# Optimization experiments

Measured on AMD Instinct MI355X. Metric: run time of the kernel, lower is better.

The kernel has to match this reference:

```python
import jax, jax.numpy as jnp
import numpy as np

B, T, N, CD, D = 8, 16, 256, 1280, 1024   # batch, frames, feats/frame, condition_dim, dim
H, DH, DEPTH, Q = 16, 64, 6, 16           # heads, dim_head, depth, latents per frame
FF = 4 * D


def setup_inputs() -> dict:
    key = jax.random.key(0)
    ks = iter(jax.random.split(key, 40))
    w = lambda shp: jax.random.normal(next(ks), shp, jnp.float32) * 0.02
    return dict(
        x_f=jax.random.normal(next(ks), (B, T, N, CD), jnp.float32),
        goal_w1=w((CD, 2 * D)), goal_b1=jnp.zeros((2 * D,), jnp.float32),
        goal_w2=w((2 * D, D)), goal_b2=jnp.zeros((D,), jnp.float32),
        latents=jax.random.normal(next(ks), (T, Q, D), jnp.float32),
        time_pos_emb=jax.random.normal(next(ks), (T, 1, D), jnp.float32),
        ln_media_g=jnp.ones((DEPTH, D), jnp.float32), ln_media_b=jnp.zeros((DEPTH, D), jnp.float32),
        ln_lat_g=jnp.ones((DEPTH, D), jnp.float32), ln_lat_b=jnp.zeros((DEPTH, D), jnp.float32),
        wq=w((DEPTH, D, H * DH)), wk=w((DEPTH, D, H * DH)), wv=w((DEPTH, D, H * DH)),
        wo=w((DEPTH, H * DH, D)),
        ffn_ln_g=jnp.ones((DEPTH, D), jnp.float32), ffn_ln_b=jnp.zeros((DEPTH, D), jnp.float32),
        ffn_w1=w((DEPTH, D, FF)), ffn_b1=jnp.zeros((DEPTH, FF), jnp.float32),
        ffn_w2=w((DEPTH, FF, D)), ffn_b2=jnp.zeros((DEPTH, D), jnp.float32),
        final_g=jnp.ones((D,), jnp.float32), final_b=jnp.zeros((D,), jnp.float32),
    )


def layer_norm(x, g, b, eps=1e-5):
    m = jnp.mean(x, axis=-1, keepdims=True)
    v = jnp.mean(jnp.square(x - m), axis=-1, keepdims=True)
    return (x - m) * jax.lax.rsqrt(v + eps) * g + b


def reference(x_f, goal_w1, goal_b1, goal_w2, goal_b2, latents, time_pos_emb,
              ln_media_g, ln_media_b, ln_lat_g, ln_lat_b, wq, wk, wv, wo,
              ffn_ln_g, ffn_ln_b, ffn_w1, ffn_b1, ffn_w2, ffn_b2, final_g, final_b):
    scale = DH ** -0.5
    # goal embedding: Linear -> GELU(exact) -> Linear, then add time positional embedding
    h = jax.nn.gelu(x_f @ goal_w1 + goal_b1, approximate=False) @ goal_w2 + goal_b2  # (B,T,N,D)
    h = h + time_pos_emb[None]                                                       # (T,1,D) broadcast
    feats = h.reshape(B * T, N, D)
    x = jnp.broadcast_to(latents[None], (B, T, Q, D)).reshape(B * T, Q, D)
    for i in range(DEPTH):
        f = layer_norm(feats, ln_media_g[i], ln_media_b[i])
        lat = layer_norm(x, ln_lat_g[i], ln_lat_b[i])
        q = (lat @ wq[i]).reshape(B * T, Q, H, DH).transpose(0, 2, 1, 3) * scale  # bhqd
        kv = jnp.concatenate([f, lat], axis=1)                                    # (BT, N+Q, D)
        k = (kv @ wk[i]).reshape(B * T, N + Q, H, DH).transpose(0, 2, 1, 3)       # bhfd
        v = (kv @ wv[i]).reshape(B * T, N + Q, H, DH).transpose(0, 2, 1, 3)
        sim = jnp.einsum('bhqd,bhfd->bhqf', q, k)
        alphas = jax.nn.softmax(sim, axis=-1)  # matches amax-subtract + softmax
        o = jnp.einsum('bhqf,bhfd->bhqd', alphas, v)
        o = o.transpose(0, 2, 1, 3).reshape(B * T, Q, H * DH)
        x = x + o @ wo[i]
        y = layer_norm(x, ffn_ln_g[i], ffn_ln_b[i])
        x = x + jax.nn.gelu(y @ ffn_w1[i] + ffn_b1[i], approximate=False) @ ffn_w2[i] + ffn_b2[i]
    x = x.reshape(B, T * Q, D)
    return layer_norm(x, final_g, final_b)
```

## Files before the change

### kernel.cpp

```cpp
#include <hip/hip_runtime.h>
#include <math.h>

#define DEV __device__ __forceinline__

typedef __attribute__((ext_vector_type(8))) short short8;
typedef __attribute__((ext_vector_type(4))) short short4v;
typedef __attribute__((ext_vector_type(4))) float f32x4;
typedef __attribute__((ext_vector_type(8))) __bf16 bf16x8;

DEV float bf2f(unsigned short u) {
    union { unsigned int i; float f; } c; c.i = ((unsigned int)u) << 16; return c.f;
}
DEV unsigned short f2bf(float f) {
    union { float f; unsigned int i; } c; c.f = f;
    unsigned int u = c.i;
    u += 0x7fffu + ((u >> 16) & 1u);
    return (unsigned short)(u >> 16);
}
DEV float gelu_exact(float x) { return 0.5f * x * (1.0f + erff(x * 0.70710678118654752f)); }

DEV f32x4 MF(bf16x8 a, bf16x8 b, f32x4 c) {
    return __builtin_amdgcn_mfma_f32_16x16x32_bf16(a, b, c, 0, 0, 0);
}

#define GLL16(g, l)                                                                   \
    __builtin_amdgcn_global_load_lds(                                                \
        (const __attribute__((address_space(1))) unsigned int*)(g),                  \
        (__attribute__((address_space(3))) unsigned int*)(l), 16, 0, 0)

#define BAR()     __builtin_amdgcn_s_barrier()
#define VMCNT(n)  asm volatile("s_waitcnt vmcnt(" #n ")" ::: "memory")
#define LGKM(n)   do { asm volatile("s_waitcnt lgkmcnt(" #n ")" ::: "memory");        \
                       __builtin_amdgcn_sched_barrier(0); } while (0)

__global__ __launch_bounds__(256)
void transpose_w(const float* __restrict__ in, unsigned short* __restrict__ out,
                 const float* __restrict__ rowscale, float uscale,
                 int K, int N, size_t inStride, size_t outStride, int scaleStride)
{
    __shared__ float tile[64][65];
    in  += (size_t)blockIdx.z * inStride;
    out += (size_t)blockIdx.z * outStride;
    const int k0 = blockIdx.y * 64, n0 = blockIdx.x * 64;
    const int tid = threadIdx.x;
    const int c = tid & 63;
#pragma unroll
    for (int i = 0; i < 16; ++i) {
        int rr = (i << 2) + (tid >> 6);
        float v = in[(size_t)(k0 + rr) * N + n0 + c];
        if (rowscale) v *= rowscale[(size_t)blockIdx.z * scaleStride + k0 + rr];
        tile[rr][c] = v * uscale;
    }
    __syncthreads();
#pragma unroll
    for (int i = 0; i < 16; ++i) {
        int rr = (i << 2) + (tid >> 6);
        out[(size_t)(n0 + rr) * K + k0 + c] = f2bf(tile[c][rr]);
    }
}

__global__ __launch_bounds__(256)
void fold_bias(const float* __restrict__ wk, const float* __restrict__ wv,
               const float* __restrict__ bmed, float* __restrict__ biaskv)
{
    const int d = blockIdx.x >> 3;
    const int rem = blockIdx.x & 7;
    const int part = rem >> 2;
    const int chunk = rem & 3;
    const float* w = (part ? wv : wk) + (size_t)d * 1024 * 1024 + chunk * 256 + threadIdx.x;
    const float* b = bmed + d * 1024;
    float acc = 0.f;
    for (int r = 0; r < 1024; ++r) acc += b[r] * w[(size_t)r * 1024];
    biaskv[d * 2048 + part * 1024 + chunk * 256 + threadIdx.x] = acc;
}

__global__ __launch_bounds__(256)
void convert_bf16(const float* __restrict__ in, unsigned short* __restrict__ out, size_t n4)
{
    size_t i = (size_t)blockIdx.x * 256 + threadIdx.x;
    if (i >= n4) return;
    float4 v = ((const float4*)in)[i];
    ushort4 u;
    u.x = f2bf(v.x); u.y = f2bf(v.y); u.z = f2bf(v.z); u.w = f2bf(v.w);
    ((ushort4*)out)[i] = u;
}

__global__ __launch_bounds__(256)
void init_x(const float* __restrict__ lat, float* __restrict__ x)
{
    const int row = blockIdx.x;
    ((float4*)x)[(size_t)row * 256 + threadIdx.x] =
        ((const float4*)lat)[(size_t)(row & 255) * 256 + threadIdx.x];
}

template<bool AFFINE, bool OUTBF>
__global__ __launch_bounds__(256)
void ln_k(const float* __restrict__ in, const float* __restrict__ g,
          const float* __restrict__ b, void* __restrict__ out)
{
    const int row = blockIdx.x;
    const int tid = threadIdx.x;
    float4 v = ((const float4*)(in + (size_t)row * 1024))[tid];
    float s  = v.x + v.y + v.z + v.w;
    float ss = v.x * v.x + v.y * v.y + v.z * v.z + v.w * v.w;
#pragma unroll
    for (int o = 32; o > 0; o >>= 1) { s += __shfl_down(s, o); ss += __shfl_down(ss, o); }
    __shared__ float red[8];
    if ((tid & 63) == 0) { red[tid >> 6] = s; red[4 + (tid >> 6)] = ss; }
    __syncthreads();
    const float sum  = red[0] + red[1] + red[2] + red[3];
    const float ssum = red[4] + red[5] + red[6] + red[7];
    const float mean = sum * (1.0f / 1024.0f);
    const float var  = ssum * (1.0f / 1024.0f) - mean * mean;
    const float rs   = rsqrtf(var + 1e-5f);
    float o0 = (v.x - mean) * rs, o1 = (v.y - mean) * rs;
    float o2 = (v.z - mean) * rs, o3 = (v.w - mean) * rs;
    if (AFFINE) {
        float4 gv = ((const float4*)g)[tid];
        float4 bv = ((const float4*)b)[tid];
        o0 = o0 * gv.x + bv.x; o1 = o1 * gv.y + bv.y;
        o2 = o2 * gv.z + bv.z; o3 = o3 * gv.w + bv.w;
    }
    if (OUTBF) {
        ushort4 u; u.x = f2bf(o0); u.y = f2bf(o1); u.z = f2bf(o2); u.w = f2bf(o3);
        ((ushort4*)out)[(size_t)row * 256 + tid] = u;
    } else {
        float4 ov; ov.x = o0; ov.y = o1; ov.z = o2; ov.w = o3;
        ((float4*)out)[(size_t)row * 256 + tid] = ov;
    }
}

enum { E_BF16 = 0, E_BIAS_BF16, E_BIAS_GELU_BF16, E_BIAS_TPOS_F32, E_ADD_F32, E_BIAS_ADD_F32 };

template<int EPI>
__global__ __launch_bounds__(512, 2)
void g8p(const unsigned short* __restrict__ A, const unsigned short* __restrict__ Bt,
         void* __restrict__ Out,
         const float* __restrict__ bias, const float* __restrict__ tpos,
         int M, int N, int K)
{
    __shared__ unsigned short sm[65536];

    const int tid = threadIdx.x;
    const int wid = tid >> 6, lane = tid & 63;
    const int wm = wid >> 2, wn = wid & 3;

    const int nbx = N >> 8;
    const int nwg = gridDim.x;
    const int bid = blockIdx.x;
    const int wg = (bid & 7) * (nwg >> 3) + (bid >> 3);
    const int by = wg / nbx, bx = wg % nbx;
    const int nt = K >> 6;

    const int srow = wid * 8 + (lane >> 3);
    const int schk = ((lane & 7) ^ (lane >> 3)) * 8;
    const unsigned short* gA = A  + (size_t)(by * 256 + srow) * K + schk;
    const unsigned short* gB = Bt + (size_t)(bx * 256 + srow) * K + schk;
    const int ldst = wid * 512;

    auto stgA = [&](int d, int h, int T) {
        const unsigned short* g = gA + (size_t)(h * 64) * K + (size_t)T * 64;
        unsigned short* l = sm + d * 16384 + h * 8192 + ldst;
        GLL16(g, l);
        GLL16(g + (size_t)128 * K, l + 4096);
    };
    auto stgB = [&](int d, int h, int T) {
        const unsigned short* g = gB + (size_t)(h * 128) * K + (size_t)T * 64;
        unsigned short* l = sm + 32768 + d * 16384 + h * 8192 + ldst;
        GLL16(g, l);
        GLL16(g + (size_t)64 * K, l + 4096);
    };

    const int q = lane >> 4;
    const int cks0 = ((q    ) ^ (lane & 7)) * 8;
    const int cks1 = ((q + 4) ^ (lane & 7)) * 8;
    const int arow = (wm * 64 + (lane & 15)) * 64;
    const int brow = ((wn & 1) * 64 + (lane & 15)) * 64;
    const int bhoff = 32768 + (wn >> 1) * 8192;

    f32x4 acc[8][4] = {};
    bf16x8 ax[2][2], ay[2][2], b[4][2];

#define READ_A(dst, base, HOFF, E0)                                                  \
    dst[0][0] = *(const bf16x8*)((base) + (HOFF) + arow + (E0) * 1024 + cks0);       \
    dst[0][1] = *(const bf16x8*)((base) + (HOFF) + arow + (E0) * 1024 + cks1);       \
    dst[1][0] = *(const bf16x8*)((base) + (HOFF) + arow + ((E0) + 1) * 1024 + cks0); \
    dst[1][1] = *(const bf16x8*)((base) + (HOFF) + arow + ((E0) + 1) * 1024 + cks1);

#define READ_Bm(Bb)                                                                  \
    _Pragma("unroll")                                                                \
    for (int ni = 0; ni < 4; ++ni) {                                                 \
        b[ni][0] = *(const bf16x8*)((Bb) + brow + ni * 1024 + cks0);                 \
        b[ni][1] = *(const bf16x8*)((Bb) + brow + ni * 1024 + cks1);                 \
    }

#define CLUST(R0, as)                                                                \
    __builtin_amdgcn_s_setprio(1);                                                   \
    _Pragma("unroll")                                                                \
    for (int e = 0; e < 2; ++e)                                                      \
        _Pragma("unroll")                                                            \
        for (int ni = 0; ni < 4; ++ni) {                                             \
            acc[(R0) + e][ni] = MF(as[e][0], b[ni][0], acc[(R0) + e][ni]);           \
            acc[(R0) + e][ni] = MF(as[e][1], b[ni][1], acc[(R0) + e][ni]);           \
        }                                                                            \
    __builtin_amdgcn_s_setprio(0);

    stgB(0, 0, 0); stgA(0, 0, 0); stgB(0, 1, 0); stgA(0, 1, 0);
    if (nt > 1) { stgB(1, 0, 1); stgA(1, 0, 1); }
    if (nt > 1) VMCNT(4); else VMCNT(0);
    BAR();
    READ_A(ax, sm, 0, 0);

    for (int T = 0; T < nt; ++T) {
        const int d = T & 1, dn = d ^ 1;
        const unsigned short* Ab  = sm + d * 16384;
        const unsigned short* Bb  = sm + bhoff + d * 16384;
        const unsigned short* AbN = sm + dn * 16384;
        const bool s1 = (T + 1 < nt), s2 = (T + 2 < nt);

        if (s1) { stgB(dn, 1, T + 1); stgA(dn, 1, T + 1); }
        READ_Bm(Bb);
        READ_A(ay, Ab, 0, 2);
        LGKM(4);
        CLUST(0, ax);
        BAR();

        if (s2) stgB(d, 0, T + 2);
        READ_A(ax, Ab, 8192, 0);
        LGKM(4);
        CLUST(2, ay);
        BAR();

        if (s2) stgA(d, 0, T + 2);
        READ_A(ay, Ab, 8192, 2);
        LGKM(4);
        CLUST(4, ax);

        if (s1) {
            if (s2) VMCNT(4); else VMCNT(0);
            BAR();
            READ_A(ax, AbN, 0, 0);
            LGKM(4);
        } else {
            LGKM(0);
        }
        CLUST(6, ay);
        BAR();
    }
#undef READ_A
#undef READ_Bm
#undef CLUST

    const int r0 = by * 256 + wm * 128 + (lane >> 4) * 4;
    const int c0 = bx * 256 + wn * 64 + (lane & 15);
#pragma unroll
    for (int mi = 0; mi < 8; ++mi) {
#pragma unroll
        for (int ni = 0; ni < 4; ++ni) {
            const int c = c0 + ni * 16;
            float bv = 0.f;
            if (EPI == E_BIAS_BF16 || EPI == E_BIAS_GELU_BF16 || EPI == E_BIAS_TPOS_F32)
                bv = bias[c];
#pragma unroll
            for (int j = 0; j < 4; ++j) {
                const int r = r0 + mi * 16 + j;
                float v = acc[mi][ni][j] + bv;
                if (EPI == E_BIAS_GELU_BF16) v = gelu_exact(v);
                if (EPI == E_BIAS_TPOS_F32) {
                    v += tpos[(((unsigned)r >> 8) & 15) * 1024 + c];
                    ((float*)Out)[(size_t)r * N + c] = v;
                } else {
                    ((unsigned short*)Out)[(size_t)r * N + c] = f2bf(v);
                }
            }
        }
    }
}

template<int EPI>
__global__ __launch_bounds__(256, 4)
void gemm64(const unsigned short* __restrict__ A, const unsigned short* __restrict__ Bt,
            void* __restrict__ Out,
            const float* __restrict__ bias, const float* __restrict__ addsrc,
            int M, int N, int K)
{
    __shared__ unsigned short lds[64 * 64 + 128 * 64];
    const int tid  = threadIdx.x;
    const int wave = tid >> 6, lane = tid & 63;
    const int nbx  = N >> 7;

    const int nwg = gridDim.x;
    int bid = blockIdx.x;
    int wg = ((nwg & 7) == 0) ? ((bid & 7) * (nwg >> 3) + (bid >> 3)) : bid;
    const int by = wg / nbx, bx = wg % nbx;

    const int swz = ((lane & 7) ^ (lane >> 3)) * 8;
    const unsigned short* gA = A  + (size_t)(by * 64  + (lane >> 3)) * K + swz;
    const unsigned short* gB = Bt + (size_t)(bx * 128 + (lane >> 3)) * K + swz;

    const int wr = wave >> 1, wc = wave & 1;
    f32x4 acc[2][4] = {};

    unsigned short* ldsA = lds;
    unsigned short* ldsB = lds + 64 * 64;

    const int off0 = (((lane >> 4)    ) ^ (lane & 7)) * 8;
    const int off1 = (((lane >> 4) | 4) ^ (lane & 7)) * 8;
    const unsigned short* la = ldsA + (wr * 32 + (lane & 15)) * 64;
    const unsigned short* lb = ldsB + (wc * 64 + (lane & 15)) * 64;

    for (int kt = 0; kt < K; kt += 64) {
        GLL16(gA + (size_t)(wave)     * 8 * K + kt, ldsA + (wave)      * 512);
        GLL16(gA + (size_t)(4 + wave) * 8 * K + kt, ldsA + (4 + wave)  * 512);
#pragma unroll
        for (int j = 0; j < 4; ++j) {
            const int chunk = (j << 2) + wave;
            GLL16(gB + (size_t)chunk * 8 * K + kt, ldsB + chunk * 512);
        }
        __syncthreads();
#pragma unroll
        for (int kk = 0; kk < 2; ++kk) {
            const int offk = kk ? off1 : off0;
            bf16x8 a[2], b[4];
#pragma unroll
            for (int m = 0; m < 2; ++m) a[m] = *(const bf16x8*)(la + m * 1024 + offk);
#pragma unroll
            for (int n = 0; n < 4; ++n) b[n] = *(const bf16x8*)(lb + n * 1024 + offk);
#pragma unroll
            for (int m = 0; m < 2; ++m)
#pragma unroll
                for (int n = 0; n < 4; ++n)
                    acc[m][n] = __builtin_amdgcn_mfma_f32_16x16x32_bf16(a[m], b[n], acc[m][n], 0, 0, 0);
        }
        __syncthreads();
    }

    const int r0 = by * 64 + wr * 32 + (lane >> 4) * 4;
    const int c0 = bx * 128 + wc * 64 + (lane & 15);
#pragma unroll
    for (int m = 0; m < 2; ++m) {
#pragma unroll
        for (int n = 0; n < 4; ++n) {
            const int c = c0 + n * 16;
#pragma unroll
            for (int j = 0; j < 4; ++j) {
                const int r = r0 + m * 16 + j;
                float v = acc[m][n][j];
                if (EPI == E_BIAS_BF16 || EPI == E_BIAS_GELU_BF16 || EPI == E_BIAS_ADD_F32)
                    v += bias[c];
                if (EPI == E_BIAS_GELU_BF16) v = gelu_exact(v);
                if (EPI == E_ADD_F32 || EPI == E_BIAS_ADD_F32) v += addsrc[(size_t)r * N + c];
                if (EPI == E_ADD_F32 || EPI == E_BIAS_ADD_F32)
                    ((float*)Out)[(size_t)r * N + c] = v;
                else
                    ((unsigned short*)Out)[(size_t)r * N + c] = f2bf(v);
            }
        }
    }
}

__global__ __launch_bounds__(256)
void attn_k(const unsigned short* __restrict__ qkvl, const unsigned short* __restrict__ kvm,
            unsigned short* __restrict__ o)
{
    __shared__ unsigned short kv[272 * 72];
    __shared__ float sim[16 * 273];
    __shared__ float qs[16 * 68];
    __shared__ float red[64];

    const int bt = blockIdx.x >> 4, h = blockIdx.x & 15;
    const int tid = threadIdx.x;
    const int lane = tid & 63, wave = tid >> 6;
    const int r = tid & 15, grp = tid >> 4;

    {
        const int qi = tid >> 4, d0 = (tid & 15) * 4;
        const unsigned short* src = qkvl + (size_t)(bt * 16 + qi) * 3072 + h * 64 + d0;
        qs[qi * 68 + d0 + 0] = bf2f(src[0]);
        qs[qi * 68 + d0 + 1] = bf2f(src[1]);
        qs[qi * 68 + d0 + 2] = bf2f(src[2]);
        qs[qi * 68 + d0 + 3] = bf2f(src[3]);
    }
#pragma unroll
    for (int i = 0; i < 9; ++i) {
        int idx = i * 256 + tid;
        if (idx < 2176) {
            int f = idx >> 3, cp = idx & 7;
            const unsigned short* src = (f < 256)
                ? kvm  + (size_t)(bt * 256 + f) * 2048 + h * 64 + cp * 8
                : qkvl + (size_t)(bt * 16 + (f - 256)) * 3072 + 1024 + h * 64 + cp * 8;
            *(short8*)&kv[f * 72 + cp * 8] = *(const short8*)src;
        }
    }
    __syncthreads();

    float p[17];
#pragma unroll
    for (int i = 0; i < 17; ++i) p[i] = 0.f;
#pragma unroll
    for (int d = 0; d < 64; d += 8) {
        float q8[8];
#pragma unroll
        for (int j = 0; j < 8; ++j) q8[j] = qs[r * 68 + d + j];
#pragma unroll
        for (int i = 0; i < 17; ++i) {
            short8 k8 = *(const short8*)&kv[(grp + i * 16) * 72 + d];
#pragma unroll
            for (int j = 0; j < 8; ++j) p[i] += q8[j] * bf2f((unsigned short)k8[j]);
        }
    }
    float mx = -3.0e38f;
#pragma unroll
    for (int i = 0; i < 17; ++i) mx = fmaxf(mx, p[i]);
    mx = fmaxf(mx, __shfl_xor(mx, 16));
    mx = fmaxf(mx, __shfl_xor(mx, 32));
    if (lane < 16) red[wave * 16 + lane] = mx;
    __syncthreads();
    const float rowmax = fmaxf(fmaxf(red[r], red[16 + r]), fmaxf(red[32 + r], red[48 + r]));

    float sm = 0.f;
#pragma unroll
    for (int i = 0; i < 17; ++i) { p[i] = __expf(p[i] - rowmax); sm += p[i]; }
    sm += __shfl_xor(sm, 16);
    sm += __shfl_xor(sm, 32);
#pragma unroll
    for (int i = 0; i < 17; ++i) sim[r * 273 + grp + i * 16] = p[i];
    __syncthreads();
    if (lane < 16) red[wave * 16 + lane] = sm;
#pragma unroll
    for (int i = 0; i < 9; ++i) {
        int idx = i * 256 + tid;
        if (idx < 2176) {
            int f = idx >> 3, cp = idx & 7;
            const unsigned short* src = (f < 256)
                ? kvm  + (size_t)(bt * 256 + f) * 2048 + 1024 + h * 64 + cp * 8
                : qkvl + (size_t)(bt * 16 + (f - 256)) * 3072 + 2048 + h * 64 + cp * 8;
            *(short8*)&kv[f * 72 + cp * 8] = *(const short8*)src;
        }
    }
    __syncthreads();
    const float inv = 1.0f / (red[r] + red[16 + r] + red[32 + r] + red[48 + r]);

    float o0 = 0.f, o1 = 0.f, o2 = 0.f, o3 = 0.f;
    for (int f = 0; f < 272; ++f) {
        float pv = sim[r * 273 + f];
        short4v v4 = *(const short4v*)&kv[f * 72 + grp * 4];
        o0 += pv * bf2f((unsigned short)v4[0]);
        o1 += pv * bf2f((unsigned short)v4[1]);
        o2 += pv * bf2f((unsigned short)v4[2]);
        o3 += pv * bf2f((unsigned short)v4[3]);
    }
    unsigned short* dst = o + (size_t)(bt * 16 + r) * 1024 + h * 64 + grp * 4;
    dst[0] = f2bf(o0 * inv);
    dst[1] = f2bf(o1 * inv);
    dst[2] = f2bf(o2 * inv);
    dst[3] = f2bf(o3 * inv);
}

extern "C" void kernel_launch(void* const* d_in, const int* in_sizes, int n_in,
                              void* d_out, int out_size, void* d_ws, size_t ws_size,
                              hipStream_t stream)
{
    const float* x_f      = (const float*)d_in[0];
    const float* goal_w1  = (const float*)d_in[1];
    const float* goal_b1  = (const float*)d_in[2];
    const float* goal_w2  = (const float*)d_in[3];
    const float* goal_b2  = (const float*)d_in[4];
    const float* latents  = (const float*)d_in[5];
    const float* tpos     = (const float*)d_in[6];
    const float* lnm_g    = (const float*)d_in[7];
    const float* lnm_b    = (const float*)d_in[8];
    const float* lnl_g    = (const float*)d_in[9];
    const float* lnl_b    = (const float*)d_in[10];
    const float* wq       = (const float*)d_in[11];
    const float* wk       = (const float*)d_in[12];
    const float* wv       = (const float*)d_in[13];
    const float* wo       = (const float*)d_in[14];
    const float* ffn_g    = (const float*)d_in[15];
    const float* ffn_b    = (const float*)d_in[16];
    const float* ffw1     = (const float*)d_in[17];
    const float* ffb1     = (const float*)d_in[18];
    const float* ffw2     = (const float*)d_in[19];
    const float* ffb2     = (const float*)d_in[20];
    const float* fin_g    = (const float*)d_in[21];
    const float* fin_b    = (const float*)d_in[22];

    char* ws = (char*)d_ws;
    size_t off = 0;
    auto alloc = [&](size_t bytes) -> char* {
        char* p = ws + off;
        off += (bytes + 255) & ~(size_t)255;
        return p;
    };
    typedef unsigned short u16;
    u16*   wg1t   = (u16*)  alloc(2048ull * 1280 * 2);
    u16*   wg2t   = (u16*)  alloc(1024ull * 2048 * 2);
    u16*   wqkvl  = (u16*)  alloc(6ull * 3072 * 1024 * 2);
    u16*   wkvm   = (u16*)  alloc(6ull * 2048 * 1024 * 2);
    u16*   wot    = (u16*)  alloc(6ull * 1024 * 1024 * 2);
    u16*   wf1t   = (u16*)  alloc(6ull * 4096 * 1024 * 2);
    u16*   wf2t   = (u16*)  alloc(6ull * 1024 * 4096 * 2);
    float* biaskv = (float*)alloc(6ull * 2048 * 4);
    float* xres   = (float*)alloc(2048ull * 1024 * 4);
    u16*   latn   = (u16*)  alloc(2048ull * 1024 * 2);
    u16*   qkvl   = (u16*)  alloc(2048ull * 3072 * 2);
    u16*   obuf   = (u16*)  alloc(2048ull * 1024 * 2);
    u16*   ffny   = (u16*)  alloc(2048ull * 1024 * 2);
    u16*   ffnmid = (u16*)  alloc(2048ull * 4096 * 2);
    u16*   bufA   = (u16*)  alloc(32768ull * 2048 * 2);
    float* bufB   = (float*)alloc(32768ull * 1024 * 4);
    u16*   bufC   = (u16*)  alloc(41943040ull * 2);
    if (off > ws_size) return;

    convert_bf16<<<40960, 256, 0, stream>>>(x_f, bufC, 41943040ull / 4);
    transpose_w<<<dim3(32, 20, 1), 256, 0, stream>>>(goal_w1, wg1t, nullptr, 1.f, 1280, 2048, 0, 0, 0);
    transpose_w<<<dim3(16, 32, 1), 256, 0, stream>>>(goal_w2, wg2t, nullptr, 1.f, 2048, 1024, 0, 0, 0);
    transpose_w<<<dim3(16, 16, 6), 256, 0, stream>>>(wq, wqkvl,                nullptr, 0.125f, 1024, 1024, 1024ull*1024, 3072ull*1024, 0);
    transpose_w<<<dim3(16, 16, 6), 256, 0, stream>>>(wk, wqkvl + 1024ull*1024, nullptr, 1.f,    1024, 1024, 1024ull*1024, 3072ull*1024, 0);
    transpose_w<<<dim3(16, 16, 6), 256, 0, stream>>>(wv, wqkvl + 2048ull*1024, nullptr, 1.f,    1024, 1024, 1024ull*1024, 3072ull*1024, 0);
    transpose_w<<<dim3(16, 16, 6), 256, 0, stream>>>(wk, wkvm,                 lnm_g,   1.f,    1024, 1024, 1024ull*1024, 2048ull*1024, 1024);
    transpose_w<<<dim3(16, 16, 6), 256, 0, stream>>>(wv, wkvm + 1024ull*1024,  lnm_g,   1.f,    1024, 1024, 1024ull*1024, 2048ull*1024, 1024);
    transpose_w<<<dim3(16, 16, 6), 256, 0, stream>>>(wo, wot,                  nullptr, 1.f,    1024, 1024, 1024ull*1024, 1024ull*1024, 0);
    transpose_w<<<dim3(64, 16, 6), 256, 0, stream>>>(ffw1, wf1t,               nullptr, 1.f,    1024, 4096, 4096ull*1024, 4096ull*1024, 0);
    transpose_w<<<dim3(16, 64, 6), 256, 0, stream>>>(ffw2, wf2t,               nullptr, 1.f,    4096, 1024, 4096ull*1024, 4096ull*1024, 0);
    fold_bias<<<48, 256, 0, stream>>>(wk, wv, lnm_b, biaskv);
    init_x<<<2048, 256, 0, stream>>>(latents, xres);

    g8p<E_BIAS_GELU_BF16><<<1024, 512, 0, stream>>>(bufC, wg1t, bufA, goal_b1, nullptr, 32768, 2048, 1280);
    g8p<E_BIAS_TPOS_F32><<<512, 512, 0, stream>>>(bufA, wg2t, bufB, goal_b2, tpos, 32768, 1024, 2048);
    ln_k<false, true><<<32768, 256, 0, stream>>>(bufB, nullptr, nullptr, bufC);

    for (int i = 0; i < 6; ++i) {
        const u16* wqkvl_i = wqkvl + (size_t)i * 3072 * 1024;
        const u16* wkvm_i  = wkvm  + (size_t)i * 2048 * 1024;
        const u16* wot_i   = wot   + (size_t)i * 1024 * 1024;
        const u16* wf1_i   = wf1t  + (size_t)i * 4096 * 1024;
        const u16* wf2_i   = wf2t  + (size_t)i * 1024 * 4096;

        ln_k<true, true><<<2048, 256, 0, stream>>>(xres, lnl_g + i * 1024, lnl_b + i * 1024, latn);
        gemm64<E_BF16><<<32 * 24, 256, 0, stream>>>(latn, wqkvl_i, qkvl, nullptr, nullptr, 2048, 3072, 1024);
        g8p<E_BIAS_BF16><<<1024, 512, 0, stream>>>(bufC, wkvm_i, bufA, biaskv + i * 2048, nullptr, 32768, 2048, 1024);
        attn_k<<<2048, 256, 0, stream>>>(qkvl, bufA, obuf);
        gemm64<E_ADD_F32><<<32 * 8, 256, 0, stream>>>(obuf, wot_i, xres, nullptr, xres, 2048, 1024, 1024);
        ln_k<true, true><<<2048, 256, 0, stream>>>(xres, ffn_g + i * 1024, ffn_b + i * 1024, ffny);
        gemm64<E_BIAS_GELU_BF16><<<32 * 32, 256, 0, stream>>>(ffny, wf1_i, ffnmid, ffb1 + i * 4096, nullptr, 2048, 4096, 1024);
        gemm64<E_BIAS_ADD_F32><<<32 * 8, 256, 0, stream>>>(ffnmid, wf2_i, xres, ffb2 + i * 1024, xres, 2048, 1024, 4096);
    }

    ln_k<true, false><<<2048, 256, 0, stream>>>(xres, fin_g, fin_b, d_out);
}
```

Before: 2.727 ms.

## Restructure GEMM main loop with ping-pong B registers and one barrier per tile

Rewrites the large-tile GEMM K-loop as a two-way unrolled TILE macro. B fragments alternate between two register sets, so the next tile's B and A can be read right after a single barrier and overlap with the last MFMA cluster. This removes the three extra barriers per tile of the old schedule. In exchange, global prefetch depth drops from two tiles ahead to one, with a full vmcnt(0) wait every tile, and register pressure rises from the extra B buffer. The unroll assumes an even tile count, which the model's K sizes satisfy.

```diff
diff --git a/kernel.cpp b/kernel.cpp
--- a/kernel.cpp
+++ b/kernel.cpp
@@ -179,7 +179,7 @@
     const int bhoff = 32768 + (wn >> 1) * 8192;
 
     f32x4 acc[8][4] = {};
-    bf16x8 ax[2][2], ay[2][2], b[4][2];
+    bf16x8 aX[2][2], aY[2][2], b0[4][2], b1[4][2];
 
 #define READ_A(dst, base, HOFF, E0)                                                  \
     dst[0][0] = *(const bf16x8*)((base) + (HOFF) + arow + (E0) * 1024 + cks0);       \
@@ -187,69 +187,70 @@
     dst[1][0] = *(const bf16x8*)((base) + (HOFF) + arow + ((E0) + 1) * 1024 + cks0); \
     dst[1][1] = *(const bf16x8*)((base) + (HOFF) + arow + ((E0) + 1) * 1024 + cks1);
 
-#define READ_Bm(Bb)                                                                  \
+#define READ_B(dst, Bb)                                                              \
     _Pragma("unroll")                                                                \
     for (int ni = 0; ni < 4; ++ni) {                                                 \
-        b[ni][0] = *(const bf16x8*)((Bb) + brow + ni * 1024 + cks0);                 \
-        b[ni][1] = *(const bf16x8*)((Bb) + brow + ni * 1024 + cks1);                 \
-    }
-
-#define CLUST(R0, as)                                                                \
+        dst[ni][0] = *(const bf16x8*)((Bb) + brow + ni * 1024 + cks0);               \
+        dst[ni][1] = *(const bf16x8*)((Bb) + brow + ni * 1024 + cks1);               \
+    }
+
+#define CLUST(R0, AS, BS)                                                            \
     __builtin_amdgcn_s_setprio(1);                                                   \
     _Pragma("unroll")                                                                \
     for (int e = 0; e < 2; ++e)                                                      \
         _Pragma("unroll")                                                            \
         for (int ni = 0; ni < 4; ++ni) {                                             \
-            acc[(R0) + e][ni] = MF(as[e][0], b[ni][0], acc[(R0) + e][ni]);           \
-            acc[(R0) + e][ni] = MF(as[e][1], b[ni][1], acc[(R0) + e][ni]);           \
+            acc[(R0) + e][ni] = MF(AS[e][0], BS[ni][0], acc[(R0) + e][ni]);          \
+            acc[(R0) + e][ni] = MF(AS[e][1], BS[ni][1], acc[(R0) + e][ni]);          \
         }                                                                            \
     __builtin_amdgcn_s_setprio(0);
 
+#define TILE(T, D, BC, BN)                                                           \
+    {                                                                                \
+        const int dn_ = (D) ^ 1;                                                     \
+        const unsigned short* Ab  = sm + (D) * 16384;                                \
+        const unsigned short* AbN = sm + dn_ * 16384;                                \
+        const unsigned short* BbN = sm + bhoff + dn_ * 16384;                        \
+        const bool s1 = ((T) + 1 < nt);                                              \
+                                                                             \
+        if (s1) { stgB(dn_, 0, (T) + 1); stgA(dn_, 0, (T) + 1); }                    \
+        READ_A(aY, Ab, 0, 2);                                                        \
+        LGKM(4);                                                                     \
+        CLUST(0, aX, BC);                                                            \
+                                                                             \
+        if (s1) { stgB(dn_, 1, (T) + 1); stgA(dn_, 1, (T) + 1); }                    \
+        READ_A(aX, Ab, 8192, 0);                                                     \
+        LGKM(4);                                                                     \
+        CLUST(2, aY, BC);                                                            \
+                                                                             \
+        READ_A(aY, Ab, 8192, 2);                                                     \
+        LGKM(4);                                                                     \
+        CLUST(4, aX, BC);                                                            \
+                                                                             \
+        LGKM(0);                                                                     \
+        if (s1) {                                                                    \
+            VMCNT(0);                                                                \
+            BAR();                                                                   \
+            READ_B(BN, BbN);                                                         \
+            READ_A(aX, AbN, 0, 0);                                                   \
+        }                                                                            \
+        CLUST(6, aY, BC);                                                            \
+    }
+
     stgB(0, 0, 0); stgA(0, 0, 0); stgB(0, 1, 0); stgA(0, 1, 0);
-    if (nt > 1) { stgB(1, 0, 1); stgA(1, 0, 1); }
-    if (nt > 1) VMCNT(4); else VMCNT(0);
+    VMCNT(0);
     BAR();
-    READ_A(ax, sm, 0, 0);
-
-    for (int T = 0; T < nt; ++T) {
-        const int d = T & 1, dn = d ^ 1;
-        const unsigned short* Ab  = sm + d * 16384;
-        const unsigned short* Bb  = sm + bhoff + d * 16384;
-        const unsigned short* AbN = sm + dn * 16384;
-        const bool s1 = (T + 1 < nt), s2 = (T + 2 < nt);
-
-        if (s1) { stgB(dn, 1, T + 1); stgA(dn, 1, T + 1); }
-        READ_Bm(Bb);
-        READ_A(ay, Ab, 0, 2);
-        LGKM(4);
-        CLUST(0, ax);
-        BAR();
-
-        if (s2) stgB(d, 0, T + 2);
-        READ_A(ax, Ab, 8192, 0);
-        LGKM(4);
-        CLUST(2, ay);
-        BAR();
-
-        if (s2) stgA(d, 0, T + 2);
-        READ_A(ay, Ab, 8192, 2);
-        LGKM(4);
-        CLUST(4, ax);
-
-        if (s1) {
-            if (s2) VMCNT(4); else VMCNT(0);
-            BAR();
-            READ_A(ax, AbN, 0, 0);
-            LGKM(4);
-        } else {
-            LGKM(0);
-        }
-        CLUST(6, ay);
-        BAR();
+    READ_B(b0, sm + bhoff);
+    READ_A(aX, sm, 0, 0);
+
+    for (int T = 0; T < nt; T += 2) {
+        TILE(T, 0, b0, b1);
+        TILE(T + 1, 1, b1, b0);
     }
 #undef READ_A
-#undef READ_Bm
+#undef READ_B
 #undef CLUST
+#undef TILE
 
     const int r0 = by * 256 + wm * 128 + (lane >> 4) * 4;
     const int c0 = bx * 256 + wn * 64 + (lane & 15);
@@ -330,7 +331,7 @@
             for (int m = 0; m < 2; ++m)
 #pragma unroll
                 for (int n = 0; n < 4; ++n)
-                    acc[m][n] = __builtin_amdgcn_mfma_f32_16x16x32_bf16(a[m], b[n], acc[m][n], 0, 0, 0);
+                    acc[m][n] = MF(a[m], b[n], acc[m][n]);
         }
         __syncthreads();
     }
```

After: 2.802 ms. 2.7% more time.
